# Performance work log

Measured on AMD Instinct MI355X. Metric: run time of the kernel, lower is better.

## Reference

```python
import jax, jax.numpy as jnp
import numpy as np
import math

HEAD = 4

def _neighbors3x3(t):
    # t: [b, g, d, h, w] -> [b, g, d, 9, h, w], zero-padded 3x3 neighborhoods
    b, g, d, h, w = t.shape
    tp = jnp.pad(t, ((0, 0), (0, 0), (0, 0), (1, 1), (1, 1)))
    # torch.nn.Unfold(kernel_size=3) ordering: kernel positions row-major (dy, dx)
    patches = [tp[:, :, :, dy:dy + h, dx:dx + w] for dy in range(3) for dx in range(3)]
    return jnp.stack(patches, axis=3)


def setup_inputs() -> dict:
    key = jax.random.key(0)
    k1, k2 = jax.random.split(key)
    x = jax.random.normal(k1, (8, 128, 96, 96), dtype=jnp.float32)
    # 1x1 conv weight, no bias: [out=3*out_features, in=in_features]
    W_trans = jax.random.normal(k2, (384, 128), dtype=jnp.float32) * 0.05
    return {"x": x, "W_trans": W_trans}


def reference(x, W_trans):
    b, cin, h, w = x.shape
    # 1x1 conv == channel GEMM
    t = jnp.einsum('bchw,oc->bohw', x, W_trans)  # [b, 3*C, h, w]
    q, k, v = jnp.split(t, 3, axis=1)            # each [b, C, h, w]
    C = q.shape[1]
    d = C // HEAD
    q = q.reshape(b, HEAD, d, h, w)
    k = k.reshape(b, HEAD, d, h, w)
    v = v.reshape(b, HEAD, d, h, w)
    kn = _neighbors3x3(k)  # [b, g, d, 9, h, w]
    vn = _neighbors3x3(v)  # [b, g, d, 9, h, w]
    # att[b,g,n,h,w] = <q[b,g,:,h,w], kn[b,g,:,n,h,w]> / sqrt(d)
    att = jnp.einsum('bgdhw,bgdnhw->bgnhw', q, kn) / math.sqrt(d)
    att = jax.nn.softmax(att, axis=2)
    # dropout p=0.4 is identity in eval mode
    out = jnp.einsum('bgnhw,bgdnhw->bgdhw', att, vn)  # [b, g, d, h, w]
    return out.reshape(b, C, h, w)
```

## Files before the change

### kernel.cpp

```cpp
#include <hip/hip_runtime.h>

#define NB     8
#define CIN    128
#define HEADS  4
#define DHEAD  32
#define HDIM   96
#define WDIM   96
#define HW     9216

#define TH     8
#define TW     16
#define HR     (TH + 2)
#define HC     (TW + 2)
#define HP     (HR * HC)
#define NT     12
#define NPOS   (NT * 16)
#define NPOSP  (NPOS + 1)
#define QP     (TH * TW)

typedef __fp16 f16x2 __attribute__((ext_vector_type(2)));
typedef __fp16 f16x8 __attribute__((ext_vector_type(8)));
typedef float  f32x4 __attribute__((ext_vector_type(4)));

__device__ __forceinline__ unsigned pkh2(float a, float b) {
  f16x2 h = __builtin_amdgcn_cvt_pkrtz(a, b);
  return *(unsigned*)&h;
}
__device__ __forceinline__ float dot2(unsigned a, unsigned b, float c) {
#if __has_builtin(__builtin_amdgcn_fdot2)
  return __builtin_amdgcn_fdot2(*(f16x2*)&a, *(f16x2*)&b, c, false);
#else
  f16x2 ha = *(f16x2*)&a, hb = *(f16x2*)&b;
  c = fmaf((float)ha[0], (float)hb[0], c);
  return fmaf((float)ha[1], (float)hb[1], c);
#endif
}

__global__ __launch_bounds__(256) void xpack_kernel(const float* __restrict__ x,
                                                    uint4* __restrict__ xT) {
  __shared__ unsigned l[64 * 67];
  const int b  = blockIdx.y;
  const int p0 = blockIdx.x * 64;
  const int t  = threadIdx.x;
  const int p  = t & 63, cg = t >> 6;
  const float* xb = x + (size_t)b * CIN * HW + p0 + p;
#pragma unroll
  for (int i = 0; i < 16; ++i) {
    const int c = cg * 32 + 2 * i;
    float f0 = xb[(size_t)c * HW];
    float f1 = xb[(size_t)(c + 1) * HW];
    l[p * 67 + cg * 16 + i] = pkh2(f0, f1);
  }
  __syncthreads();
  uint4* dst = xT + ((size_t)b * HW + p0) * 16;
#pragma unroll
  for (int k = 0; k < 4; ++k) {
    const int u = k * 256 + t;
    const int pos = u >> 4, ch = u & 15;
    uint4 d;
    d.x = l[pos * 67 + ch * 4 + 0];
    d.y = l[pos * 67 + ch * 4 + 1];
    d.z = l[pos * 67 + ch * 4 + 2];
    d.w = l[pos * 67 + ch * 4 + 3];
    dst[u] = d;
  }
}

__global__ __launch_bounds__(256) void wpack_kernel(const float* __restrict__ W,
                                                    uint4* __restrict__ Wf) {
  const int u = blockIdx.x * 256 + threadIdx.x;
  const int lane = u & 63, kb = (u >> 6) & 3, otp = u >> 8;
  const int g = otp / 6, r = otp % 6, s = r >> 1, ph = r & 1;
  const int o = (s * 8 + g * 2 + ph) * 16 + (lane & 15);
  const int c0 = kb * 32 + (lane >> 4) * 8;
  const float4* w = (const float4*)(W + (size_t)o * CIN + c0);
  float4 w0 = w[0], w1 = w[1];
  uint4 rr;
  rr.x = pkh2(w0.x, w0.y); rr.y = pkh2(w0.z, w0.w);
  rr.z = pkh2(w1.x, w1.y); rr.w = pkh2(w1.z, w1.w);
  Wf[u] = rr;
}

__global__ __launch_bounds__(256, 4) void fused_kernel(const uint4* __restrict__ xT,
                                                       const uint4* __restrict__ Wf,
                                                       float* __restrict__ out) {
  __shared__ uint4 qs[4 * QP];
  __shared__ uint4 ks[4 * NPOSP];
  __shared__ uint4 vs[4 * NPOSP];

  const int z  = blockIdx.z;
  const int b  = z >> 1, hpair = z & 1;
  const int h0 = blockIdx.y * TH;
  const int w0 = blockIdx.x * TW;
  const int t  = threadIdx.x;
  const int wv = t >> 6, lane = t & 63;
  const int colp = lane & 15, quad = lane >> 4;

  uint4 frags[3][4];
  {
    const size_t xb16 = (size_t)b * HW * 16;
#pragma unroll
    for (int i = 0; i < 3; ++i) {
      const int hp = (wv * 3 + i) * 16 + colp;
      const int hr = hp / HC, hc = hp - hr * HC;
      const int hh = h0 - 1 + hr, ww = w0 - 1 + hc;
      const bool ok = (hp < HP) & (hh >= 0) & (hh < HDIM) & (ww >= 0) & (ww < WDIM);
#pragma unroll
      for (int kb = 0; kb < 4; ++kb) {
        uint4 r = {0u, 0u, 0u, 0u};
        if (ok)
          r = xT[xb16 + (size_t)(hh * WDIM + ww) * 16 + kb * 4 + quad];
        frags[i][kb] = r;
      }
    }
  }

  const int pos = t & 127, dh = t >> 7;
  const int y = pos >> 4, xx = pos & 15;
  const int pbase = (y + 1) * HC + (xx + 1);

#pragma unroll 1
  for (int gi = 0; gi < 2; ++gi) {
    const int g = hpair * 2 + gi;
    if (gi) __syncthreads();

#pragma unroll
    for (int s = 0; s < 3; ++s) {
#pragma unroll
      for (int ph = 0; ph < 2; ++ph) {
        const int otp = g * 6 + s * 2 + ph;
        f16x8 af[4];
#pragma unroll
        for (int kb = 0; kb < 4; ++kb) {
          uint4 tmp = Wf[(otp * 4 + kb) * 64 + lane];
          af[kb] = *(f16x8*)&tmp;
        }
        const int d0 = ph * 16 + quad * 4;
#pragma unroll
        for (int i = 0; i < 3; ++i) {
          f32x4 acc = {0.f, 0.f, 0.f, 0.f};
#pragma unroll
          for (int kb = 0; kb < 4; ++kb)
            acc = __builtin_amdgcn_mfma_f32_16x16x32_f16(
                af[kb], *(f16x8*)&frags[i][kb], acc, 0, 0, 0);
          const int pw = (wv * 3 + i) * 16 + colp;
          uint2 st;
          st.x = pkh2(acc[0], acc[1]);
          st.y = pkh2(acc[2], acc[3]);
          if (s == 0) {
            const int hr = pw / HC, hc = pw - hr * HC;
            if (((unsigned)(hr - 1) < TH) & ((unsigned)(hc - 1) < TW)) {
              const int idx = (hr - 1) * TW + (hc - 1);
              *(uint2*)((unsigned short*)(qs + (d0 >> 3) * QP + idx)
                        + ((d0 >> 2) & 1) * 4) = st;
            }
          } else {
            uint4* dst = (s == 1) ? ks : vs;
            *(uint2*)((unsigned short*)(dst + (d0 >> 3) * NPOSP + pw)
                      + ((d0 >> 2) & 1) * 4) = st;
          }
        }
      }
    }
    __syncthreads();

    unsigned qp[16];
#pragma unroll
    for (int c = 0; c < 4; ++c) {
      uint4 u = qs[c * QP + pos];
      qp[c * 4 + 0] = u.x; qp[c * 4 + 1] = u.y;
      qp[c * 4 + 2] = u.z; qp[c * 4 + 3] = u.w;
    }

    float att[9];
#pragma unroll
    for (int nn = 0; nn < 9; ++nn) {
      const int pn = pbase + (nn / 3 - 1) * HC + (nn % 3 - 1);
      float dot = 0.0f;
#pragma unroll
      for (int c = 0; c < 4; ++c) {
        uint4 ku = ks[c * NPOSP + pn];
        dot = dot2(qp[c * 4 + 0], ku.x, dot);
        dot = dot2(qp[c * 4 + 1], ku.y, dot);
        dot = dot2(qp[c * 4 + 2], ku.z, dot);
        dot = dot2(qp[c * 4 + 3], ku.w, dot);
      }
      att[nn] = dot * 0.17677669529663687f;
    }

    float m = att[0];
#pragma unroll
    for (int nn = 1; nn < 9; ++nn) m = fmaxf(m, att[nn]);
    float ssum = 0.0f;
#pragma unroll
    for (int nn = 0; nn < 9; ++nn) { att[nn] = __expf(att[nn] - m); ssum += att[nn]; }
    const float inv = 1.0f / ssum;

    float acc[16];
#pragma unroll
    for (int i = 0; i < 16; ++i) acc[i] = 0.0f;
#pragma unroll
    for (int nn = 0; nn < 9; ++nn) {
      const float wn = att[nn] * inv;
      const int pn = pbase + (nn / 3 - 1) * HC + (nn % 3 - 1);
#pragma unroll
      for (int cc = 0; cc < 2; ++cc) {
        uint4 vv = vs[(dh * 2 + cc) * NPOSP + pn];
        f16x2 h0 = *(f16x2*)&vv.x, h1 = *(f16x2*)&vv.y;
        f16x2 h2 = *(f16x2*)&vv.z, h3 = *(f16x2*)&vv.w;
        acc[cc * 8 + 0] = fmaf(wn, (float)h0[0], acc[cc * 8 + 0]);
        acc[cc * 8 + 1] = fmaf(wn, (float)h0[1], acc[cc * 8 + 1]);
        acc[cc * 8 + 2] = fmaf(wn, (float)h1[0], acc[cc * 8 + 2]);
        acc[cc * 8 + 3] = fmaf(wn, (float)h1[1], acc[cc * 8 + 3]);
        acc[cc * 8 + 4] = fmaf(wn, (float)h2[0], acc[cc * 8 + 4]);
        acc[cc * 8 + 5] = fmaf(wn, (float)h2[1], acc[cc * 8 + 5]);
        acc[cc * 8 + 6] = fmaf(wn, (float)h3[0], acc[cc * 8 + 6]);
        acc[cc * 8 + 7] = fmaf(wn, (float)h3[1], acc[cc * 8 + 7]);
      }
    }

    float* ob = out + ((size_t)b * CIN + (size_t)g * DHEAD + (size_t)dh * 16) * HW
              + (size_t)(h0 + y) * WDIM + (w0 + xx);
#pragma unroll
    for (int i = 0; i < 16; ++i) ob[(size_t)i * HW] = acc[i];
  }
}

extern "C" void kernel_launch(void* const* d_in, const int* in_sizes, int n_in,
                              void* d_out, int out_size, void* d_ws, size_t ws_size,
                              hipStream_t stream) {
  (void)in_sizes; (void)n_in; (void)out_size; (void)ws_size;
  const float* x = (const float*)d_in[0];
  const float* W = (const float*)d_in[1];
  float* out = (float*)d_out;

  uint4* xT = (uint4*)d_ws;
  uint4* Wf = (uint4*)((char*)d_ws + (size_t)NB * HW * 256);

  xpack_kernel<<<dim3(HW / 64, NB), 256, 0, stream>>>(x, xT);
  wpack_kernel<<<24, 256, 0, stream>>>(W, Wf);
  fused_kernel<<<dim3(WDIM / TW, HDIM / TH, NB * 2), 256, 0, stream>>>(xT, Wf, out);
}
```

Measured before the change: 119.8 us.

## Split fused kernel to one head per block and merge pack kernels

```diff
diff --git a/kernel.cpp b/kernel.cpp
--- a/kernel.cpp
+++ b/kernel.cpp
@@ -15,7 +15,6 @@
 #define HP     (HR * HC)
 #define NT     12
 #define NPOS   (NT * 16)
-#define NPOSP  (NPOS + 1)
 #define QP     (TH * TW)
 
 typedef __fp16 f16x2 __attribute__((ext_vector_type(2)));
@@ -36,60 +35,64 @@
 #endif
 }
 
-__global__ __launch_bounds__(256) void xpack_kernel(const float* __restrict__ x,
-                                                    uint4* __restrict__ xT) {
+#define XBLKS (NB * (HW / 64))
+
+__global__ __launch_bounds__(256) void prep_kernel(const float* __restrict__ x,
+                                                   const float* __restrict__ W,
+                                                   uint4* __restrict__ xT,
+                                                   uint4* __restrict__ Wf) {
   __shared__ unsigned l[64 * 67];
-  const int b  = blockIdx.y;
-  const int p0 = blockIdx.x * 64;
-  const int t  = threadIdx.x;
-  const int p  = t & 63, cg = t >> 6;
-  const float* xb = x + (size_t)b * CIN * HW + p0 + p;
-#pragma unroll
-  for (int i = 0; i < 16; ++i) {
-    const int c = cg * 32 + 2 * i;
-    float f0 = xb[(size_t)c * HW];
-    float f1 = xb[(size_t)(c + 1) * HW];
-    l[p * 67 + cg * 16 + i] = pkh2(f0, f1);
-  }
-  __syncthreads();
-  uint4* dst = xT + ((size_t)b * HW + p0) * 16;
-#pragma unroll
-  for (int k = 0; k < 4; ++k) {
-    const int u = k * 256 + t;
-    const int pos = u >> 4, ch = u & 15;
-    uint4 d;
-    d.x = l[pos * 67 + ch * 4 + 0];
-    d.y = l[pos * 67 + ch * 4 + 1];
-    d.z = l[pos * 67 + ch * 4 + 2];
-    d.w = l[pos * 67 + ch * 4 + 3];
-    dst[u] = d;
-  }
-}
-
-__global__ __launch_bounds__(256) void wpack_kernel(const float* __restrict__ W,
-                                                    uint4* __restrict__ Wf) {
-  const int u = blockIdx.x * 256 + threadIdx.x;
-  const int lane = u & 63, kb = (u >> 6) & 3, otp = u >> 8;
-  const int g = otp / 6, r = otp % 6, s = r >> 1, ph = r & 1;
-  const int o = (s * 8 + g * 2 + ph) * 16 + (lane & 15);
-  const int c0 = kb * 32 + (lane >> 4) * 8;
-  const float4* w = (const float4*)(W + (size_t)o * CIN + c0);
-  float4 w0 = w[0], w1 = w[1];
-  uint4 rr;
-  rr.x = pkh2(w0.x, w0.y); rr.y = pkh2(w0.z, w0.w);
-  rr.z = pkh2(w1.x, w1.y); rr.w = pkh2(w1.z, w1.w);
-  Wf[u] = rr;
-}
-
-__global__ __launch_bounds__(256, 4) void fused_kernel(const uint4* __restrict__ xT,
+  const int bid = blockIdx.x;
+  const int t   = threadIdx.x;
+  if (bid < XBLKS) {
+    const int b  = bid / (HW / 64);
+    const int p0 = (bid % (HW / 64)) * 64;
+    const int p  = t & 63, cg = t >> 6;
+    const float* xb = x + (size_t)b * CIN * HW + p0 + p;
+#pragma unroll
+    for (int i = 0; i < 16; ++i) {
+      const int c = cg * 32 + 2 * i;
+      float f0 = xb[(size_t)c * HW];
+      float f1 = xb[(size_t)(c + 1) * HW];
+      l[p * 67 + cg * 16 + i] = pkh2(f0, f1);
+    }
+    __syncthreads();
+    uint4* dst = xT + ((size_t)b * HW + p0) * 16;
+#pragma unroll
+    for (int k = 0; k < 4; ++k) {
+      const int u = k * 256 + t;
+      const int pos = u >> 4, ch = u & 15;
+      uint4 d;
+      d.x = l[pos * 67 + ch * 4 + 0];
+      d.y = l[pos * 67 + ch * 4 + 1];
+      d.z = l[pos * 67 + ch * 4 + 2];
+      d.w = l[pos * 67 + ch * 4 + 3];
+      dst[u] = d;
+    }
+  } else {
+    const int u = (bid - XBLKS) * 256 + t;
+    const int lane = u & 63, kb = (u >> 6) & 3, otp = u >> 8;
+    const int g = otp / 6, r = otp % 6, s = r >> 1, ph = r & 1;
+    const int o = (s * 8 + g * 2 + ph) * 16 + (lane & 15);
+    const int c0 = kb * 32 + (lane >> 4) * 8;
+    const float4* w = (const float4*)(W + (size_t)o * CIN + c0);
+    float4 w0 = w[0], w1 = w[1];
+    uint4 rr;
+    rr.x = pkh2(w0.x, w0.y); rr.y = pkh2(w0.z, w0.w);
+    rr.z = pkh2(w1.x, w1.y); rr.w = pkh2(w1.z, w1.w);
+    Wf[u] = rr;
+  }
+}
+
+__global__ __launch_bounds__(256, 5) void fused_kernel(const uint4* __restrict__ xT,
                                                        const uint4* __restrict__ Wf,
                                                        float* __restrict__ out) {
   __shared__ uint4 qs[4 * QP];
-  __shared__ uint4 ks[4 * NPOSP];
-  __shared__ uint4 vs[4 * NPOSP];
+  __shared__ uint4 ks[4 * NPOS];
+  __shared__ uint4 vs[4 * NPOS];
 
   const int z  = blockIdx.z;
-  const int b  = z >> 1, hpair = z & 1;
+  const int b  = z >> 2, g = z & 3;
   const int h0 = blockIdx.y * TH;
   const int w0 = blockIdx.x * TW;
   const int t  = threadIdx.x;
@@ -115,115 +118,109 @@
     }
   }
 
+#pragma unroll
+  for (int s = 0; s < 3; ++s) {
+#pragma unroll
+    for (int ph = 0; ph < 2; ++ph) {
+      const int otp = g * 6 + s * 2 + ph;
+      f16x8 af[4];
+#pragma unroll
+      for (int kb = 0; kb < 4; ++kb) {
+        uint4 tmp = Wf[(otp * 4 + kb) * 64 + lane];
+        af[kb] = *(f16x8*)&tmp;
+      }
+      const int d0 = ph * 16 + quad * 4;
+#pragma unroll
+      for (int i = 0; i < 3; ++i) {
+        f32x4 acc = {0.f, 0.f, 0.f, 0.f};
+#pragma unroll
+        for (int kb = 0; kb < 4; ++kb)
+          acc = __builtin_amdgcn_mfma_f32_16x16x32_f16(
+              af[kb], *(f16x8*)&frags[i][kb], acc, 0, 0, 0);
+        const int pw = (wv * 3 + i) * 16 + colp;
+        uint2 st;
+        st.x = pkh2(acc[0], acc[1]);
+        st.y = pkh2(acc[2], acc[3]);
+        if (s == 0) {
+          const int hr = pw / HC, hc = pw - hr * HC;
+          if (((unsigned)(hr - 1) < TH) & ((unsigned)(hc - 1) < TW)) {
+            const int idx = (hr - 1) * TW + (hc - 1);
+            *(uint2*)((unsigned short*)(qs + (d0 >> 3) * QP + idx)
+                      + ((d0 >> 2) & 1) * 4) = st;
+          }
+        } else {
+          uint4* dst = (s == 1) ? ks : vs;
+          *(uint2*)((unsigned short*)(dst + (d0 >> 3) * NPOS + pw)
+                    + ((d0 >> 2) & 1) * 4) = st;
+        }
+      }
+    }
+  }
+  __syncthreads();
+
   const int pos = t & 127, dh = t >> 7;
   const int y = pos >> 4, xx = pos & 15;
   const int pbase = (y + 1) * HC + (xx + 1);
 
-#pragma unroll 1
-  for (int gi = 0; gi < 2; ++gi) {
-    const int g = hpair * 2 + gi;
-    if (gi) __syncthreads();
-
-#pragma unroll
-    for (int s = 0; s < 3; ++s) {
-#pragma unroll
-      for (int ph = 0; ph < 2; ++ph) {
-        const int otp = g * 6 + s * 2 + ph;
-        f16x8 af[4];
-#pragma unroll
-        for (int kb = 0; kb < 4; ++kb) {
-          uint4 tmp = Wf[(otp * 4 + kb) * 64 + lane];
-          af[kb] = *(f16x8*)&tmp;
-        }
-        const int d0 = ph * 16 + quad * 4;
-#pragma unroll
-        for (int i = 0; i < 3; ++i) {
-          f32x4 acc = {0.f, 0.f, 0.f, 0.f};
-#pragma unroll
-          for (int kb = 0; kb < 4; ++kb)
-            acc = __builtin_amdgcn_mfma_f32_16x16x32_f16(
-                af[kb], *(f16x8*)&frags[i][kb], acc, 0, 0, 0);
-          const int pw = (wv * 3 + i) * 16 + colp;
-          uint2 st;
-          st.x = pkh2(acc[0], acc[1]);
-          st.y = pkh2(acc[2], acc[3]);
-          if (s == 0) {
-            const int hr = pw / HC, hc = pw - hr * HC;
-            if (((unsigned)(hr - 1) < TH) & ((unsigned)(hc - 1) < TW)) {
-              const int idx = (hr - 1) * TW + (hc - 1);
-              *(uint2*)((unsigned short*)(qs + (d0 >> 3) * QP + idx)
-                        + ((d0 >> 2) & 1) * 4) = st;
-            }
-          } else {
-            uint4* dst = (s == 1) ? ks : vs;
-            *(uint2*)((unsigned short*)(dst + (d0 >> 3) * NPOSP + pw)
-                      + ((d0 >> 2) & 1) * 4) = st;
-          }
-        }
-      }
-    }
-    __syncthreads();
-
-    unsigned qp[16];
+  unsigned qp[16];
+#pragma unroll
+  for (int c = 0; c < 4; ++c) {
+    uint4 u = qs[c * QP + pos];
+    qp[c * 4 + 0] = u.x; qp[c * 4 + 1] = u.y;
+    qp[c * 4 + 2] = u.z; qp[c * 4 + 3] = u.w;
+  }
+
+  float att[9];
+#pragma unroll
+  for (int nn = 0; nn < 9; ++nn) {
+    const int pn = pbase + (nn / 3 - 1) * HC + (nn % 3 - 1);
+    float dot = 0.0f;
 #pragma unroll
     for (int c = 0; c < 4; ++c) {
-      uint4 u = qs[c * QP + pos];
-      qp[c * 4 + 0] = u.x; qp[c * 4 + 1] = u.y;
-      qp[c * 4 + 2] = u.z; qp[c * 4 + 3] = u.w;
-    }
-
-    float att[9];
-#pragma unroll
-    for (int nn = 0; nn < 9; ++nn) {
-      const int pn = pbase + (nn / 3 - 1) * HC + (nn % 3 - 1);
-      float dot = 0.0f;
-#pragma unroll
-      for (int c = 0; c < 4; ++c) {
-        uint4 ku = ks[c * NPOSP + pn];
-        dot = dot2(qp[c * 4 + 0], ku.x, dot);
-        dot = dot2(qp[c * 4 + 1], ku.y, dot);
-        dot = dot2(qp[c * 4 + 2], ku.z, dot);
-        dot = dot2(qp[c * 4 + 3], ku.w, dot);
-      }
-      att[nn] = dot * 0.17677669529663687f;
-    }
-
-    float m = att[0];
-#pragma unroll
-    for (int nn = 1; nn < 9; ++nn) m = fmaxf(m, att[nn]);
-    float ssum = 0.0f;
-#pragma unroll
-    for (int nn = 0; nn < 9; ++nn) { att[nn] = __expf(att[nn] - m); ssum += att[nn]; }
-    const float inv = 1.0f / ssum;
-
-    float acc[16];
-#pragma unroll
-    for (int i = 0; i < 16; ++i) acc[i] = 0.0f;
-#pragma unroll
-    for (int nn = 0; nn < 9; ++nn) {
-      const float wn = att[nn] * inv;
-      const int pn = pbase + (nn / 3 - 1) * HC + (nn % 3 - 1);
-#pragma unroll
-      for (int cc = 0; cc < 2; ++cc) {
-        uint4 vv = vs[(dh * 2 + cc) * NPOSP + pn];
-        f16x2 h0 = *(f16x2*)&vv.x, h1 = *(f16x2*)&vv.y;
-        f16x2 h2 = *(f16x2*)&vv.z, h3 = *(f16x2*)&vv.w;
-        acc[cc * 8 + 0] = fmaf(wn, (float)h0[0], acc[cc * 8 + 0]);
-        acc[cc * 8 + 1] = fmaf(wn, (float)h0[1], acc[cc * 8 + 1]);
-        acc[cc * 8 + 2] = fmaf(wn, (float)h1[0], acc[cc * 8 + 2]);
-        acc[cc * 8 + 3] = fmaf(wn, (float)h1[1], acc[cc * 8 + 3]);
-        acc[cc * 8 + 4] = fmaf(wn, (float)h2[0], acc[cc * 8 + 4]);
-        acc[cc * 8 + 5] = fmaf(wn, (float)h2[1], acc[cc * 8 + 5]);
-        acc[cc * 8 + 6] = fmaf(wn, (float)h3[0], acc[cc * 8 + 6]);
-        acc[cc * 8 + 7] = fmaf(wn, (float)h3[1], acc[cc * 8 + 7]);
-      }
-    }
-
-    float* ob = out + ((size_t)b * CIN + (size_t)g * DHEAD + (size_t)dh * 16) * HW
-              + (size_t)(h0 + y) * WDIM + (w0 + xx);
-#pragma unroll
-    for (int i = 0; i < 16; ++i) ob[(size_t)i * HW] = acc[i];
-  }
+      uint4 ku = ks[c * NPOS + pn];
+      dot = dot2(qp[c * 4 + 0], ku.x, dot);
+      dot = dot2(qp[c * 4 + 1], ku.y, dot);
+      dot = dot2(qp[c * 4 + 2], ku.z, dot);
+      dot = dot2(qp[c * 4 + 3], ku.w, dot);
+    }
+    att[nn] = dot * 0.17677669529663687f;
+  }
+
+  float m = att[0];
+#pragma unroll
+  for (int nn = 1; nn < 9; ++nn) m = fmaxf(m, att[nn]);
+  float ssum = 0.0f;
+#pragma unroll
+  for (int nn = 0; nn < 9; ++nn) { att[nn] = __expf(att[nn] - m); ssum += att[nn]; }
+  const float inv = 1.0f / ssum;
+
+  float acc[16];
+#pragma unroll
+  for (int i = 0; i < 16; ++i) acc[i] = 0.0f;
+#pragma unroll
+  for (int nn = 0; nn < 9; ++nn) {
+    const float wn = att[nn] * inv;
+    const int pn = pbase + (nn / 3 - 1) * HC + (nn % 3 - 1);
+#pragma unroll
+    for (int cc = 0; cc < 2; ++cc) {
+      uint4 vv = vs[(dh * 2 + cc) * NPOS + pn];
+      f16x2 h0 = *(f16x2*)&vv.x, h1 = *(f16x2*)&vv.y;
+      f16x2 h2 = *(f16x2*)&vv.z, h3 = *(f16x2*)&vv.w;
+      acc[cc * 8 + 0] = fmaf(wn, (float)h0[0], acc[cc * 8 + 0]);
+      acc[cc * 8 + 1] = fmaf(wn, (float)h0[1], acc[cc * 8 + 1]);
+      acc[cc * 8 + 2] = fmaf(wn, (float)h1[0], acc[cc * 8 + 2]);
+      acc[cc * 8 + 3] = fmaf(wn, (float)h1[1], acc[cc * 8 + 3]);
+      acc[cc * 8 + 4] = fmaf(wn, (float)h2[0], acc[cc * 8 + 4]);
+      acc[cc * 8 + 5] = fmaf(wn, (float)h2[1], acc[cc * 8 + 5]);
+      acc[cc * 8 + 6] = fmaf(wn, (float)h3[0], acc[cc * 8 + 6]);
+      acc[cc * 8 + 7] = fmaf(wn, (float)h3[1], acc[cc * 8 + 7]);
+    }
+  }
+
+  float* ob = out + ((size_t)b * CIN + (size_t)g * DHEAD + (size_t)dh * 16) * HW
+            + (size_t)(h0 + y) * WDIM + (w0 + xx);
+#pragma unroll
+  for (int i = 0; i < 16; ++i) ob[(size_t)i * HW] = acc[i];
 }
 
 extern "C" void kernel_launch(void* const* d_in, const int* in_sizes, int n_in,
@@ -237,7 +234,6 @@
   uint4* xT = (uint4*)d_ws;
   uint4* Wf = (uint4*)((char*)d_ws + (size_t)NB * HW * 256);
 
-  xpack_kernel<<<dim3(HW / 64, NB), 256, 0, stream>>>(x, xT);
-  wpack_kernel<<<24, 256, 0, stream>>>(W, Wf);
-  fused_kernel<<<dim3(WDIM / TW, HDIM / TH, NB * 2), 256, 0, stream>>>(xT, Wf, out);
-}
+  prep_kernel<<<XBLKS + 24, 256, 0, stream>>>(x, W, xT, Wf);
+  fused_kernel<<<dim3(WDIM / TW, HDIM / TH, NB * HEADS), 256, 0, stream>>>(xT, Wf, out);
+}
```

After: 116.7 us. -2.6%, faster.
